# Optimization experiments

Measured on AMD Instinct MI355X. Metric: run time of the kernel, lower is better.

## Reference

```python
import jax, jax.numpy as jnp
import numpy as np

# Dims
B, S, D = 4, 4096, 1024
H, NB, A = 4, 4096, 4          # hashes, buckets, associativity
DK, DV, DT = 64, 128, 32        # key dim, value (mem) dim, vsa tag dim
BITS = 12                       # log2(NB)
TEMP = 1.0
VSA_W = 1.0
TANH_SCALE = 1.0
ETA = 0.1
WRITE_THR = 0.5
MATCH_THR = 0.0
NOV_THR = 0.0
EPS = 1e-6


def _l2n(x):
    return x / (jnp.linalg.norm(x, axis=-1, keepdims=True) + EPS)


def setup_inputs() -> dict:
    key = jax.random.key(0)
    ks = jax.random.split(key, 13)
    sc = 0.02
    return {
        "u": jax.random.normal(ks[0], (B, S, D), jnp.float32),
        "memK": jax.random.normal(ks[1], (H, NB, A, DK), jnp.float32),
        "memV": jax.random.normal(ks[2], (H, NB, A, DV), jnp.float32),
        "memT": jnp.tanh(jax.random.normal(ks[3], (H, NB, A, DT), jnp.float32)),
        "Wq": jax.random.normal(ks[4], (DK, D), jnp.float32) * sc,
        "Wwk": jax.random.normal(ks[5], (DK, D), jnp.float32) * sc,
        "Wv": jax.random.normal(ks[6], (DV, D), jnp.float32) * sc,
        "Wo": jax.random.normal(ks[7], (D, DV), jnp.float32) * sc,
        "Wg": jax.random.normal(ks[8], (1, D), jnp.float32) * sc,
        "bg": jnp.zeros((1,), jnp.float32),
        "Wvsa": jax.random.normal(ks[9], (DK, DT), jnp.float32) * sc,
        "R": jax.random.normal(ks[10], (H, DK, BITS), jnp.float32),
    }


def reference(u, memK, memV, memT, Wq, Wwk, Wv, Wo, Wg, bg, Wvsa, R):
    N = B * S
    uf = u.reshape(N, D)

    # ---- routing: sign-bit LSH over query key -> bucket index per hash ----
    qkey = uf @ Wq.T                                     # [N, DK]
    bits = (jnp.einsum("nd,hdk->nhk", qkey, R) > 0).astype(jnp.int32)
    pw = (2 ** jnp.arange(BITS, dtype=jnp.int32))
    idx = (bits * pw).sum(-1)                            # [N, H] bucket ids
    hh = jnp.arange(H)[None, :]                          # [1, H]

    # ---- associative gather read ----
    Kg = memK[hh, idx]                                   # [N, H, A, DK]
    Vg = memV[hh, idx]                                   # [N, H, A, DV]
    Tg = memT[hh, idx]                                   # [N, H, A, DT]
    qtag = jnp.tanh(TANH_SCALE * (qkey @ Wvsa))          # [N, DT]
    sc = (jnp.einsum("nd,nhad->nha", qkey, Kg) / np.sqrt(DK)
          + VSA_W * jnp.einsum("nt,nhat->nha", qtag, Tg) / np.sqrt(DT))
    w = jax.nn.softmax(sc.reshape(N, H * A) / TEMP, axis=-1)
    read = jnp.einsum("nk,nkd->nd", w, Vg.reshape(N, H * A, DV))
    y = (read @ Wo.T).reshape(B, S, D)

    # ---- gated scatter write with EMA + novelty ----
    wkey = uf @ Wwk.T                                    # [N, DK]
    wval = uf @ Wv.T                                     # [N, DV]
    gate = jax.nn.sigmoid(uf @ Wg.T + bg)                # [N, 1]
    wmask = (gate > WRITE_THR).astype(u.dtype)           # [N, 1]
    wtag = jnp.tanh(TANH_SCALE * (wkey @ Wvsa))          # [N, DT]

    sim = jnp.einsum("nd,nhad->nha", _l2n(wkey), _l2n(Kg))   # [N,H,A]
    astar = jnp.argmax(sim, axis=-1)                         # [N,H]
    bsim = jnp.max(sim, axis=-1)                             # [N,H]
    take = lambda G: jnp.take_along_axis(G, astar[:, :, None, None], axis=2)[:, :, 0]
    Kbest, Vbest, Tbest = take(Kg), take(Vg), take(Tg)       # [N,H,·]

    tagsim = jnp.einsum("nt,nhat->nha", _l2n(wtag), _l2n(Tg))
    novelty = 1.0 - jnp.max(tagsim, axis=-1)                 # [N,H]

    eff = (ETA * gate * wmask
           * (bsim >= MATCH_THR).astype(u.dtype)
           * (novelty >= NOV_THR).astype(u.dtype))           # [N,H]

    dK = eff[..., None] * (wkey[:, None, :] - Kbest)
    dV = eff[..., None] * (wval[:, None, :] - Vbest)
    dT = eff[..., None] * (wtag[:, None, :] - Tbest)
    Knew = memK.at[hh, idx, astar].add(dK)
    Vnew = memV.at[hh, idx, astar].add(dV)
    Tnew = memT.at[hh, idx, astar].add(dT)
    return y, Knew, Vnew, Tnew
```

## Files before the change

kernel.cpp:

```cpp
#include <hip/hip_runtime.h>
#include <hip/hip_bf16.h>
#include <math.h>

#define NTOK    16384
#define DMODEL  1024
#define HN      4
#define NBUCKET 4096
#define ASSOC   4
#define DKEY    64
#define DVAL    128
#define DTAG    32
#define NBITS   12
#define EPSV    1e-6f

typedef __bf16 bf16x8 __attribute__((ext_vector_type(8)));
typedef float  f32x4  __attribute__((ext_vector_type(4)));
typedef float  f32x2  __attribute__((ext_vector_type(2)));

__device__ __forceinline__ unsigned short f2bf_raw(float f) {
    __hip_bfloat16 h = __float2bfloat16(f);
    return *(unsigned short*)&h;
}

__global__ __launch_bounds__(256) void gemm_mfma(const float* __restrict__ A,
                                                 const float* __restrict__ B,
                                                 float* __restrict__ C,
                                                 int M, int N, int K) {
    __shared__ __align__(16) unsigned short As[4][128][8];
    __shared__ __align__(16) unsigned short Bs[4][128][8];
    const int t    = threadIdx.x;
    const int lane = t & 63;
    const int w    = t >> 6;
    const int wm   = (w & 1) * 64;
    const int wn   = (w >> 1) * 64;
    const int bm   = blockIdx.x * 128;
    const int bn   = blockIdx.y * 128;

    const int srow = t & 127;
    const int skg  = t >> 7;
    const float* Ap = A + (size_t)(bm + srow) * K;
    const float* Bp = B + (size_t)(bn + srow) * K;

    const int fr = lane & 15;
    const int kq = lane >> 4;

    f32x4 acc[4][4] = {};

    for (int k0 = 0; k0 < K; k0 += 32) {
        #pragma unroll
        for (int ii = 0; ii < 2; ++ii) {
            const int kg = skg + ii * 2;
            const float4 a0 = *(const float4*)(Ap + k0 + kg * 8);
            const float4 a1 = *(const float4*)(Ap + k0 + kg * 8 + 4);
            const float4 b0 = *(const float4*)(Bp + k0 + kg * 8);
            const float4 b1 = *(const float4*)(Bp + k0 + kg * 8 + 4);
            unsigned short* da = &As[kg][srow][0];
            da[0] = f2bf_raw(a0.x); da[1] = f2bf_raw(a0.y);
            da[2] = f2bf_raw(a0.z); da[3] = f2bf_raw(a0.w);
            da[4] = f2bf_raw(a1.x); da[5] = f2bf_raw(a1.y);
            da[6] = f2bf_raw(a1.z); da[7] = f2bf_raw(a1.w);
            unsigned short* db = &Bs[kg][srow][0];
            db[0] = f2bf_raw(b0.x); db[1] = f2bf_raw(b0.y);
            db[2] = f2bf_raw(b0.z); db[3] = f2bf_raw(b0.w);
            db[4] = f2bf_raw(b1.x); db[5] = f2bf_raw(b1.y);
            db[6] = f2bf_raw(b1.z); db[7] = f2bf_raw(b1.w);
        }
        __syncthreads();
        bf16x8 af[4], bfv[4];
        #pragma unroll
        for (int i = 0; i < 4; ++i) af[i]  = *(const bf16x8*)&As[kq][wm + i * 16 + fr][0];
        #pragma unroll
        for (int j = 0; j < 4; ++j) bfv[j] = *(const bf16x8*)&Bs[kq][wn + j * 16 + fr][0];
        #pragma unroll
        for (int i = 0; i < 4; ++i)
            #pragma unroll
            for (int j = 0; j < 4; ++j)
                acc[i][j] = __builtin_amdgcn_mfma_f32_16x16x32_bf16(af[i], bfv[j], acc[i][j], 0, 0, 0);
        __syncthreads();
    }
    #pragma unroll
    for (int i = 0; i < 4; ++i)
        #pragma unroll
        for (int j = 0; j < 4; ++j)
            #pragma unroll
            for (int r = 0; r < 4; ++r)
                C[(size_t)(bm + wm + i * 16 + kq * 4 + r) * N + (bn + wn + j * 16 + fr)] = acc[i][j][r];
}

__global__ __launch_bounds__(256) void gemm_wval_splitk(const float* __restrict__ A,
                                                        const float* __restrict__ B,
                                                        float* __restrict__ Cpart) {
    __shared__ __align__(16) unsigned short As[4][128][8];
    __shared__ __align__(16) unsigned short Bs[4][128][8];
    const int t    = threadIdx.x;
    const int lane = t & 63;
    const int w    = t >> 6;
    const int wm   = (w & 1) * 64;
    const int wn   = (w >> 1) * 64;
    const int bm   = blockIdx.x * 128;
    const int kz   = blockIdx.y;
    const int kbeg = kz * 256;

    const int srow = t & 127;
    const int skg  = t >> 7;
    const float* Ap = A + (size_t)(bm + srow) * DMODEL;
    const float* Bp = B + (size_t)srow * DMODEL;

    const int fr = lane & 15;
    const int kq = lane >> 4;

    f32x4 acc[4][4] = {};

    for (int k0 = kbeg; k0 < kbeg + 256; k0 += 32) {
        #pragma unroll
        for (int ii = 0; ii < 2; ++ii) {
            const int kg = skg + ii * 2;
            const float4 a0 = *(const float4*)(Ap + k0 + kg * 8);
            const float4 a1 = *(const float4*)(Ap + k0 + kg * 8 + 4);
            const float4 b0 = *(const float4*)(Bp + k0 + kg * 8);
            const float4 b1 = *(const float4*)(Bp + k0 + kg * 8 + 4);
            unsigned short* da = &As[kg][srow][0];
            da[0] = f2bf_raw(a0.x); da[1] = f2bf_raw(a0.y);
            da[2] = f2bf_raw(a0.z); da[3] = f2bf_raw(a0.w);
            da[4] = f2bf_raw(a1.x); da[5] = f2bf_raw(a1.y);
            da[6] = f2bf_raw(a1.z); da[7] = f2bf_raw(a1.w);
            unsigned short* db = &Bs[kg][srow][0];
            db[0] = f2bf_raw(b0.x); db[1] = f2bf_raw(b0.y);
            db[2] = f2bf_raw(b0.z); db[3] = f2bf_raw(b0.w);
            db[4] = f2bf_raw(b1.x); db[5] = f2bf_raw(b1.y);
            db[6] = f2bf_raw(b1.z); db[7] = f2bf_raw(b1.w);
        }
        __syncthreads();
        bf16x8 af[4], bfv[4];
        #pragma unroll
        for (int i = 0; i < 4; ++i) af[i]  = *(const bf16x8*)&As[kq][wm + i * 16 + fr][0];
        #pragma unroll
        for (int j = 0; j < 4; ++j) bfv[j] = *(const bf16x8*)&Bs[kq][wn + j * 16 + fr][0];
        #pragma unroll
        for (int i = 0; i < 4; ++i)
            #pragma unroll
            for (int j = 0; j < 4; ++j)
                acc[i][j] = __builtin_amdgcn_mfma_f32_16x16x32_bf16(af[i], bfv[j], acc[i][j], 0, 0, 0);
        __syncthreads();
    }
    float* Cp = Cpart + (size_t)kz * NTOK * 128;
    #pragma unroll
    for (int i = 0; i < 4; ++i)
        #pragma unroll
        for (int j = 0; j < 4; ++j)
            #pragma unroll
            for (int r = 0; r < 4; ++r)
                Cp[(size_t)(bm + wm + i * 16 + kq * 4 + r) * 128 + (wn + j * 16 + fr)] = acc[i][j][r];
}

__global__ __launch_bounds__(256) void gemm_f32_splitk(const float* __restrict__ A,
                                                       const float* __restrict__ B,
                                                       float* __restrict__ Cpart,
                                                       int M, int K, int K_quarter) {
    __shared__ __align__(16) float As[2][16][68];
    __shared__ __align__(16) float Bs[2][16][140];
    const int t  = threadIdx.x;
    const int bm = blockIdx.x * 64;
    const int kz = blockIdx.z;
    const int tx = t & 15;
    const int ty = t >> 4;

    const int arow = t >> 2, ac = (t & 3) * 4;
    const int brow = t >> 1, bc = (t & 1) * 8;
    const int bperm = brow + ((brow >> 5) << 2);
    const int goff  = tx * 8 + ((tx >> 2) << 2);

    const float* Apt = A + (size_t)(bm + arow) * K + ac;
    const float* Bpt = B + (size_t)brow * K + bc;

    const int kbeg = kz * K_quarter;
    const int NSTEP = 16;

    f32x2 acc2[4][4] = {};

    float4 av = *(const float4*)(Apt + kbeg);
    float4 b0 = *(const float4*)(Bpt + kbeg);
    float4 b1 = *(const float4*)(Bpt + kbeg + 4);
    As[0][ac + 0][arow] = av.x; As[0][ac + 1][arow] = av.y;
    As[0][ac + 2][arow] = av.z; As[0][ac + 3][arow] = av.w;
    Bs[0][bc + 0][bperm] = b0.x; Bs[0][bc + 1][bperm] = b0.y;
    Bs[0][bc + 2][bperm] = b0.z; Bs[0][bc + 3][bperm] = b0.w;
    Bs[0][bc + 4][bperm] = b1.x; Bs[0][bc + 5][bperm] = b1.y;
    Bs[0][bc + 6][bperm] = b1.z; Bs[0][bc + 7][bperm] = b1.w;
    __syncthreads();

    for (int s = 0; s < NSTEP; ++s) {
        const int cur = s & 1;
        if (s + 1 < NSTEP) {
            const int k0 = kbeg + (s + 1) * 16;
            av = *(const float4*)(Apt + k0);
            b0 = *(const float4*)(Bpt + k0);
            b1 = *(const float4*)(Bpt + k0 + 4);
        }
        #pragma unroll
        for (int kk = 0; kk < 16; ++kk) {
            const float4 a4 = *(const float4*)&As[cur][kk][ty * 4];
            const float4 v0 = *(const float4*)&Bs[cur][kk][goff];
            const float4 v1 = *(const float4*)&Bs[cur][kk][goff + 4];
            const float aa[4] = {a4.x, a4.y, a4.z, a4.w};
            const f32x2 bb[4] = {{v0.x, v0.y}, {v0.z, v0.w}, {v1.x, v1.y}, {v1.z, v1.w}};
            #pragma unroll
            for (int i = 0; i < 4; ++i) {
                const f32x2 as2 = {aa[i], aa[i]};
                #pragma unroll
                for (int j = 0; j < 4; ++j)
                    acc2[i][j] = __builtin_elementwise_fma(as2, bb[j], acc2[i][j]);
            }
        }
        if (s + 1 < NSTEP) {
            const int nb = cur ^ 1;
            As[nb][ac + 0][arow] = av.x; As[nb][ac + 1][arow] = av.y;
            As[nb][ac + 2][arow] = av.z; As[nb][ac + 3][arow] = av.w;
            Bs[nb][bc + 0][bperm] = b0.x; Bs[nb][bc + 1][bperm] = b0.y;
            Bs[nb][bc + 2][bperm] = b0.z; Bs[nb][bc + 3][bperm] = b0.w;
            Bs[nb][bc + 4][bperm] = b1.x; Bs[nb][bc + 5][bperm] = b1.y;
            Bs[nb][bc + 6][bperm] = b1.z; Bs[nb][bc + 7][bperm] = b1.w;
        }
        __syncthreads();
    }

    float* Cp = Cpart + (size_t)kz * M * 128;
    #pragma unroll
    for (int i = 0; i < 4; ++i) {
        float4 o0, o1;
        o0.x = acc2[i][0].x; o0.y = acc2[i][0].y; o0.z = acc2[i][1].x; o0.w = acc2[i][1].y;
        o1.x = acc2[i][2].x; o1.y = acc2[i][2].y; o1.z = acc2[i][3].x; o1.w = acc2[i][3].y;
        float* dst = &Cp[(size_t)(bm + ty * 4 + i) * 128 + tx * 8];
        *(float4*)dst       = o0;
        *(float4*)(dst + 4) = o1;
    }
}

__global__ __launch_bounds__(256) void gate_kernel(const float* __restrict__ u,
                                                   const float* __restrict__ Wg,
                                                   const float* __restrict__ bg,
                                                   float* __restrict__ gateg) {
    const int wv = threadIdx.x >> 6, lane = threadIdx.x & 63;
    const int n = blockIdx.x * 4 + wv;
    const float* up = u + (size_t)n * DMODEL;
    float acc = 0.f;
    #pragma unroll
    for (int j = 0; j < 16; ++j)
        acc += up[lane + 64 * j] * Wg[lane + 64 * j];
    #pragma unroll
    for (int off = 1; off < 64; off <<= 1) acc += __shfl_xor(acc, off);
    if (lane == 0) gateg[n] = 1.f / (1.f + expf(-(acc + bg[0])));
}

__global__ __launch_bounds__(256) void route_kernel(
    const float* __restrict__ memK, const float* __restrict__ memV,
    const float* __restrict__ memT, const float* __restrict__ R,
    const float* __restrict__ Wvsa,
    const float* __restrict__ partQ, const float* __restrict__ partW,
    const float* __restrict__ gateg,
    float* __restrict__ accK, float* __restrict__ accV, float* __restrict__ accT,
    float* __restrict__ readw) {
    __shared__ float sQK[4][64], sWK[4][64], sQT[4][32], sWT[4][32];
    __shared__ float sSc[4][16], sSim[4][16], sTsim[4][16], sW[4][16];
    __shared__ int   sIdx[4][4], sAst[4][4];
    __shared__ float sEff[4][4];

    const int wv = threadIdx.x >> 6;
    const int lane = threadIdx.x & 63;
    const int n = blockIdx.x * 4 + wv;
    const size_t PZ = (size_t)NTOK * 128;

    const size_t qb = (size_t)n * 128;
    const float qk = (partQ[qb + lane]          + partQ[PZ + qb + lane])
                   + (partQ[2 * PZ + qb + lane] + partQ[3 * PZ + qb + lane]);
    const float wk = (partQ[qb + 64 + lane]          + partQ[PZ + qb + 64 + lane])
                   + (partQ[2 * PZ + qb + 64 + lane] + partQ[3 * PZ + qb + 64 + lane]);
    sQK[wv][lane] = qk;
    sWK[wv][lane] = wk;
    float wk2 = wk * wk;
    #pragma unroll
    for (int off = 1; off < 64; off <<= 1) wk2 += __shfl_xor(wk2, off);
    const float wknorm = sqrtf(wk2) + EPSV;
    const float gate = gateg[n];
    __syncthreads();

    {
        const int tg = lane & 31;
        const float* keyp = (lane < 32) ? sQK[wv] : sWK[wv];
        float tacc = 0.f;
        for (int d = 0; d < 64; ++d) tacc += keyp[d] * Wvsa[d * DTAG + tg];
        const float tagv = tanhf(tacc);
        if (lane < 32) sQT[wv][tg] = tagv; else sWT[wv][tg] = tagv;
        float wt2 = (lane >= 32) ? tagv * tagv : 0.f;
        #pragma unroll
        for (int off = 1; off < 64; off <<= 1) wt2 += __shfl_xor(wt2, off);
        const float wtnorm = sqrtf(wt2) + EPSV;

        bool bit = false;
        if (lane < 48) {
            const int h = lane / 12, k = lane % 12;
            float bacc = 0.f;
            for (int d = 0; d < 64; ++d)
                bacc += sQK[wv][d] * R[(size_t)(h * DKEY + d) * NBITS + k];
            bit = bacc > 0.f;
        }
        const unsigned long long mask = __ballot(bit);
        if (lane < 4) sIdx[wv][lane] = (int)((mask >> (12 * lane)) & 0xFFFull);
        __syncthreads();

        const int slot = lane >> 2, sub = lane & 3;
        const int sh = slot >> 2, sa = slot & 3;
        const int rowS = (sh * NBUCKET + sIdx[wv][sh]) * ASSOC + sa;
        const float* Kp = memK + (size_t)rowS * DKEY;
        const float* Tp = memT + (size_t)rowS * DTAG;
        float d_qk = 0, d_wk = 0, d_kk = 0, d_qt = 0, d_wt = 0, d_tt = 0;
        for (int j = 0; j < 16; ++j) {
            const int d = sub * 16 + j;
            const float kv = Kp[d];
            d_qk += sQK[wv][d] * kv;
            d_wk += sWK[wv][d] * kv;
            d_kk += kv * kv;
        }
        for (int j = 0; j < 8; ++j) {
            const int d = sub * 8 + j;
            const float tv = Tp[d];
            d_qt += sQT[wv][d] * tv;
            d_wt += sWT[wv][d] * tv;
            d_tt += tv * tv;
        }
        #pragma unroll
        for (int off = 1; off <= 2; off <<= 1) {
            d_qk += __shfl_xor(d_qk, off);
            d_wk += __shfl_xor(d_wk, off);
            d_kk += __shfl_xor(d_kk, off);
            d_qt += __shfl_xor(d_qt, off);
            d_wt += __shfl_xor(d_wt, off);
            d_tt += __shfl_xor(d_tt, off);
        }
        if (sub == 0) {
            sSc[wv][slot]   = d_qk * 0.125f + d_qt * 0.17677669529663687f;
            sSim[wv][slot]  = d_wk / (wknorm * (sqrtf(d_kk) + EPSV));
            sTsim[wv][slot] = d_wt / (wtnorm * (sqrtf(d_tt) + EPSV));
        }
    }
    __syncthreads();

    if (lane < 16) {
        const float sc = sSc[wv][lane];
        float m = sc;
        #pragma unroll
        for (int off = 1; off < 16; off <<= 1) m = fmaxf(m, __shfl_xor(m, off, 16));
        const float e = expf(sc - m);
        float ssum = e;
        #pragma unroll
        for (int off = 1; off < 16; off <<= 1) ssum += __shfl_xor(ssum, off, 16);
        sW[wv][lane] = e / ssum;
    }
    if (lane < 4) {
        float bs = -1e30f; int as = 0; float mt = -1e30f;
        #pragma unroll
        for (int aa = 0; aa < 4; ++aa) {
            const float sv = sSim[wv][lane * 4 + aa];
            if (sv > bs) { bs = sv; as = aa; }
            mt = fmaxf(mt, sTsim[wv][lane * 4 + aa]);
        }
        const float novelty = 1.f - mt;
        float e = 0.1f * gate;
        if (!(gate > 0.5f) || !(bs >= 0.f) || !(novelty >= 0.f)) e = 0.f;
        sEff[wv][lane] = e;
        sAst[wv][lane] = as;
    }
    __syncthreads();

    float r0 = 0.f, r1 = 0.f;
    #pragma unroll
    for (int s2 = 0; s2 < 16; ++s2) {
        const int hh = s2 >> 2, aa = s2 & 3;
        const int rw = (hh * NBUCKET + sIdx[wv][hh]) * ASSOC + aa;
        const float wgt = sW[wv][s2];
        const float* Vp = memV + (size_t)rw * DVAL;
        r0 += wgt * Vp[lane];
        r1 += wgt * Vp[64 + lane];
    }
    readw[(size_t)n * DVAL + lane]      = r0;
    readw[(size_t)n * DVAL + 64 + lane] = r1;

    const float wv0 = (partW[qb + lane]          + partW[PZ + qb + lane])
                    + (partW[2 * PZ + qb + lane] + partW[3 * PZ + qb + lane]);
    const float wv1 = (partW[qb + 64 + lane]          + partW[PZ + qb + 64 + lane])
                    + (partW[2 * PZ + qb + 64 + lane] + partW[3 * PZ + qb + 64 + lane]);
    for (int hh = 0; hh < 4; ++hh) {
        const float e = sEff[wv][hh];
        if (e == 0.f) continue;
        const int rw = (hh * NBUCKET + sIdx[wv][hh]) * ASSOC + sAst[wv][hh];
        atomicAdd(&accK[(size_t)rw * DKEY + lane],
                  e * (sWK[wv][lane] - memK[(size_t)rw * DKEY + lane]));
        atomicAdd(&accV[(size_t)rw * DVAL + lane],
                  e * (wv0 - memV[(size_t)rw * DVAL + lane]));
        atomicAdd(&accV[(size_t)rw * DVAL + 64 + lane],
                  e * (wv1 - memV[(size_t)rw * DVAL + 64 + lane]));
        if (lane < 32)
            atomicAdd(&accT[(size_t)rw * DTAG + lane],
                      e * (sWT[wv][lane] - memT[(size_t)rw * DTAG + lane]));
    }
}

extern "C" void kernel_launch(void* const* d_in, const int* in_sizes, int n_in,
                              void* d_out, int out_size, void* d_ws, size_t ws_size,
                              hipStream_t stream) {
    const float* u    = (const float*)d_in[0];
    const float* memK = (const float*)d_in[1];
    const float* memV = (const float*)d_in[2];
    const float* memT = (const float*)d_in[3];
    const float* Wq   = (const float*)d_in[4];
    const float* Wwk  = (const float*)d_in[5];
    const float* Wv   = (const float*)d_in[6];
    const float* Wo   = (const float*)d_in[7];
    const float* Wg   = (const float*)d_in[8];
    const float* bg   = (const float*)d_in[9];
    const float* Wvsa = (const float*)d_in[10];
    const float* R    = (const float*)d_in[11];

    const int nK = HN * NBUCKET * ASSOC * DKEY;
    const int nV = HN * NBUCKET * ASSOC * DVAL;
    const int nT = HN * NBUCKET * ASSOC * DTAG;

    float* y_out = (float*)d_out;
    float* K_out = y_out + (size_t)NTOK * DMODEL;
    float* V_out = K_out + nK;
    float* T_out = V_out + nV;

    float* readw = (float*)d_ws;
    float* qwW   = readw + (size_t)NTOK * 128;
    float* gateg = qwW   + (size_t)128 * DMODEL;

    float* partQ = y_out;
    float* partW = y_out + (size_t)4 * NTOK * 128;

    hipMemcpyAsync(qwW,          Wq,  (size_t)DKEY * DMODEL * 4, hipMemcpyDeviceToDevice, stream);
    hipMemcpyAsync(qwW + 65536,  Wwk, (size_t)DKEY * DMODEL * 4, hipMemcpyDeviceToDevice, stream);

    gemm_f32_splitk<<<dim3(NTOK / 64, 1, 4), 256, 0, stream>>>(u, qwW, partQ, NTOK, DMODEL, DMODEL / 4);

    gate_kernel<<<NTOK / 4, 256, 0, stream>>>(u, Wg, bg, gateg);

    gemm_wval_splitk<<<dim3(NTOK / 128, 4), 256, 0, stream>>>(u, Wv, partW);

    hipMemcpyAsync(K_out, memK, (size_t)nK * 4, hipMemcpyDeviceToDevice, stream);
    hipMemcpyAsync(V_out, memV, (size_t)nV * 4, hipMemcpyDeviceToDevice, stream);
    hipMemcpyAsync(T_out, memT, (size_t)nT * 4, hipMemcpyDeviceToDevice, stream);

    route_kernel<<<NTOK / 4, 256, 0, stream>>>(memK, memV, memT, R, Wvsa,
                                               partQ, partW, gateg,
                                               K_out, V_out, T_out, readw);

    gemm_mfma<<<dim3(NTOK / 128, DMODEL / 128), 256, 0, stream>>>(readw, Wo, y_out, NTOK, DMODEL, DVAL);
}
```

Measured before the change: 402.8 us.

## Merge memory copies into one kernel and drop split-K for the value projection

The five device-to-device memcpys (Wq, Wwk, memK, memV, memT) become a single grid-stride float4 copy kernel. The value-projection GEMM goes from 4-way split-K with partial buffers to a full-K 64-row-tile kernel with 512 threads that writes the final result to workspace, and the route kernel reads it directly instead of summing four partials. This cuts partial-buffer traffic and memcpy launch overhead. The cost is fewer MFMAs per wave, more barriers per output tile, and 256 blocks for the GEMM instead of 512.

```diff
diff --git a/kernel.cpp b/kernel.cpp
--- a/kernel.cpp
+++ b/kernel.cpp
@@ -87,70 +87,61 @@
                 C[(size_t)(bm + wm + i * 16 + kq * 4 + r) * N + (bn + wn + j * 16 + fr)] = acc[i][j][r];
 }
 
-__global__ __launch_bounds__(256) void gemm_wval_splitk(const float* __restrict__ A,
-                                                        const float* __restrict__ B,
-                                                        float* __restrict__ Cpart) {
-    __shared__ __align__(16) unsigned short As[4][128][8];
+__global__ __launch_bounds__(512) void gemm_wval64(const float* __restrict__ A,
+                                                   const float* __restrict__ B,
+                                                   float* __restrict__ wvalg) {
+    __shared__ __align__(16) unsigned short As[4][64][8];
     __shared__ __align__(16) unsigned short Bs[4][128][8];
     const int t    = threadIdx.x;
     const int lane = t & 63;
     const int w    = t >> 6;
-    const int wm   = (w & 1) * 64;
-    const int wn   = (w >> 1) * 64;
-    const int bm   = blockIdx.x * 128;
-    const int kz   = blockIdx.y;
-    const int kbeg = kz * 256;
-
-    const int srow = t & 127;
-    const int skg  = t >> 7;
-    const float* Ap = A + (size_t)(bm + srow) * DMODEL;
-    const float* Bp = B + (size_t)srow * DMODEL;
+    const int wr   = w >> 1;
+    const int wc   = w & 1;
+    const int bm   = blockIdx.x * 64;
+
+    const int arow = t >> 3;
+    const int a4   = t & 7;
+    const int brow = t >> 2;
+    const int b4p  = (t & 3) * 2;
+
+    const float* Ap = A + (size_t)(bm + arow) * DMODEL + a4 * 4;
+    const float* Bp = B + (size_t)brow * DMODEL;
 
     const int fr = lane & 15;
     const int kq = lane >> 4;
 
-    f32x4 acc[4][4] = {};
-
-    for (int k0 = kbeg; k0 < kbeg + 256; k0 += 32) {
+    f32x4 acc[4] = {};
+
+    for (int k0 = 0; k0 < DMODEL; k0 += 32) {
+        {
+            const float4 av = *(const float4*)(Ap + k0);
+            unsigned short* da = &As[a4 >> 1][arow][(a4 & 1) * 4];
+            da[0] = f2bf_raw(av.x); da[1] = f2bf_raw(av.y);
+            da[2] = f2bf_raw(av.z); da[3] = f2bf_raw(av.w);
+        }
         #pragma unroll
         for (int ii = 0; ii < 2; ++ii) {
-            const int kg = skg + ii * 2;
-            const float4 a0 = *(const float4*)(Ap + k0 + kg * 8);
-            const float4 a1 = *(const float4*)(Ap + k0 + kg * 8 + 4);
-            const float4 b0 = *(const float4*)(Bp + k0 + kg * 8);
-            const float4 b1 = *(const float4*)(Bp + k0 + kg * 8 + 4);
-            unsigned short* da = &As[kg][srow][0];
-            da[0] = f2bf_raw(a0.x); da[1] = f2bf_raw(a0.y);
-            da[2] = f2bf_raw(a0.z); da[3] = f2bf_raw(a0.w);
-            da[4] = f2bf_raw(a1.x); da[5] = f2bf_raw(a1.y);
-            da[6] = f2bf_raw(a1.z); da[7] = f2bf_raw(a1.w);
-            unsigned short* db = &Bs[kg][srow][0];
-            db[0] = f2bf_raw(b0.x); db[1] = f2bf_raw(b0.y);
-            db[2] = f2bf_raw(b0.z); db[3] = f2bf_raw(b0.w);
-            db[4] = f2bf_raw(b1.x); db[5] = f2bf_raw(b1.y);
-            db[6] = f2bf_raw(b1.z); db[7] = f2bf_raw(b1.w);
-        }
-        __syncthreads();
-        bf16x8 af[4], bfv[4];
-        #pragma unroll
-        for (int i = 0; i < 4; ++i) af[i]  = *(const bf16x8*)&As[kq][wm + i * 16 + fr][0];
-        #pragma unroll
-        for (int j = 0; j < 4; ++j) bfv[j] = *(const bf16x8*)&Bs[kq][wn + j * 16 + fr][0];
-        #pragma unroll
-        for (int i = 0; i < 4; ++i)
-            #pragma unroll
-            for (int j = 0; j < 4; ++j)
-                acc[i][j] = __builtin_amdgcn_mfma_f32_16x16x32_bf16(af[i], bfv[j], acc[i][j], 0, 0, 0);
-        __syncthreads();
-    }
-    float* Cp = Cpart + (size_t)kz * NTOK * 128;
-    #pragma unroll
-    for (int i = 0; i < 4; ++i)
+            const int b4 = b4p + ii;
+            const float4 bv = *(const float4*)(Bp + k0 + b4 * 4);
+            unsigned short* db = &Bs[b4 >> 1][brow][(b4 & 1) * 4];
+            db[0] = f2bf_raw(bv.x); db[1] = f2bf_raw(bv.y);
+            db[2] = f2bf_raw(bv.z); db[3] = f2bf_raw(bv.w);
+        }
+        __syncthreads();
+        const bf16x8 af = *(const bf16x8*)&As[kq][wr * 16 + fr][0];
+        bf16x8 bfv[4];
+        #pragma unroll
+        for (int j = 0; j < 4; ++j) bfv[j] = *(const bf16x8*)&Bs[kq][wc * 64 + j * 16 + fr][0];
         #pragma unroll
         for (int j = 0; j < 4; ++j)
-            #pragma unroll
-            for (int r = 0; r < 4; ++r)
-                Cp[(size_t)(bm + wm + i * 16 + kq * 4 + r) * 128 + (wn + j * 16 + fr)] = acc[i][j][r];
+            acc[j] = __builtin_amdgcn_mfma_f32_16x16x32_bf16(af, bfv[j], acc[j], 0, 0, 0);
+        __syncthreads();
+    }
+    #pragma unroll
+    for (int j = 0; j < 4; ++j)
+        #pragma unroll
+        for (int r = 0; r < 4; ++r)
+            wvalg[(size_t)(bm + wr * 16 + kq * 4 + r) * 128 + wc * 64 + j * 16 + fr] = acc[j][r];
 }
 
 __global__ __launch_bounds__(256) void gemm_f32_splitk(const float* __restrict__ A,
@@ -252,11 +243,30 @@
     if (lane == 0) gateg[n] = 1.f / (1.f + expf(-(acc + bg[0])));
 }
 
+__global__ __launch_bounds__(256) void copyall_kernel(
+    const float4* __restrict__ sK, const float4* __restrict__ sV,
+    const float4* __restrict__ sT, const float4* __restrict__ sWq,
+    const float4* __restrict__ sWwk,
+    float4* __restrict__ dKVT, float4* __restrict__ dW) {
+    const int nK4 = (HN * NBUCKET * ASSOC * DKEY) / 4;
+    const int nV4 = (HN * NBUCKET * ASSOC * DVAL) / 4;
+    const int nT4 = (HN * NBUCKET * ASSOC * DTAG) / 4;
+    const int nW4 = (DKEY * DMODEL) / 4;
+    const int e1 = nK4, e2 = e1 + nV4, e3 = e2 + nT4, e4 = e3 + nW4, e5 = e4 + nW4;
+    for (int i = blockIdx.x * 256 + threadIdx.x; i < e5; i += gridDim.x * 256) {
+        if (i < e1)      dKVT[i] = sK[i];
+        else if (i < e2) dKVT[i] = sV[i - e1];
+        else if (i < e3) dKVT[i] = sT[i - e2];
+        else if (i < e4) dW[i - e3] = sWq[i - e3];
+        else             dW[i - e3] = sWwk[i - e4];
+    }
+}
+
 __global__ __launch_bounds__(256) void route_kernel(
     const float* __restrict__ memK, const float* __restrict__ memV,
     const float* __restrict__ memT, const float* __restrict__ R,
     const float* __restrict__ Wvsa,
-    const float* __restrict__ partQ, const float* __restrict__ partW,
+    const float* __restrict__ partQ, const float* __restrict__ wvalg,
     const float* __restrict__ gateg,
     float* __restrict__ accK, float* __restrict__ accV, float* __restrict__ accT,
     float* __restrict__ readw) {
@@ -385,10 +395,8 @@
     readw[(size_t)n * DVAL + lane]      = r0;
     readw[(size_t)n * DVAL + 64 + lane] = r1;
 
-    const float wv0 = (partW[qb + lane]          + partW[PZ + qb + lane])
-                    + (partW[2 * PZ + qb + lane] + partW[3 * PZ + qb + lane]);
-    const float wv1 = (partW[qb + 64 + lane]          + partW[PZ + qb + 64 + lane])
-                    + (partW[2 * PZ + qb + 64 + lane] + partW[3 * PZ + qb + 64 + lane]);
+    const float wv0 = wvalg[(size_t)n * DVAL + lane];
+    const float wv1 = wvalg[(size_t)n * DVAL + 64 + lane];
     for (int hh = 0; hh < 4; ++hh) {
         const float e = sEff[wv][hh];
         if (e == 0.f) continue;
@@ -431,27 +439,25 @@
     float* T_out = V_out + nV;
 
     float* readw = (float*)d_ws;
-    float* qwW   = readw + (size_t)NTOK * 128;
+    float* wvalg = readw + (size_t)NTOK * 128;
+    float* qwW   = wvalg + (size_t)NTOK * 128;
     float* gateg = qwW   + (size_t)128 * DMODEL;
 
     float* partQ = y_out;
-    float* partW = y_out + (size_t)4 * NTOK * 128;
-
-    hipMemcpyAsync(qwW,          Wq,  (size_t)DKEY * DMODEL * 4, hipMemcpyDeviceToDevice, stream);
-    hipMemcpyAsync(qwW + 65536,  Wwk, (size_t)DKEY * DMODEL * 4, hipMemcpyDeviceToDevice, stream);
+
+    copyall_kernel<<<2048, 256, 0, stream>>>((const float4*)memK, (const float4*)memV,
+                                             (const float4*)memT, (const float4*)Wq,
+                                             (const float4*)Wwk,
+                                             (float4*)K_out, (float4*)qwW);
 
     gemm_f32_splitk<<<dim3(NTOK / 64, 1, 4), 256, 0, stream>>>(u, qwW, partQ, NTOK, DMODEL, DMODEL / 4);
 
     gate_kernel<<<NTOK / 4, 256, 0, stream>>>(u, Wg, bg, gateg);
 
-    gemm_wval_splitk<<<dim3(NTOK / 128, 4), 256, 0, stream>>>(u, Wv, partW);
-
-    hipMemcpyAsync(K_out, memK, (size_t)nK * 4, hipMemcpyDeviceToDevice, stream);
-    hipMemcpyAsync(V_out, memV, (size_t)nV * 4, hipMemcpyDeviceToDevice, stream);
-    hipMemcpyAsync(T_out, memT, (size_t)nT * 4, hipMemcpyDeviceToDevice, stream);
+    gemm_wval64<<<NTOK / 64, 512, 0, stream>>>(u, Wv, wvalg);
 
     route_kernel<<<NTOK / 4, 256, 0, stream>>>(memK, memV, memT, R, Wvsa,
-                                               partQ, partW, gateg,
+                                               partQ, wvalg, gateg,
                                                K_out, V_out, T_out, readw);
 
     gemm_mfma<<<dim3(NTOK / 128, DMODEL / 128), 256, 0, stream>>>(readw, Wo, y_out, NTOK, DMODEL, DVAL);
```

Result: no change. 406.1 us (+0.8%).

## Fuse query/write-key and value projections into one interleaved kernel without split-K for values

Applied to the files above, without the earlier changes.

Merges the fp32 split-K query/write-key GEMM and the bf16 MFMA value GEMM into a single launch of 1280 blocks, interleaving one value-projection block among every four key-projection blocks so the two workloads share the GPU. The value projection now runs over the full K=1024 per 64-row tile and writes final results directly, which removes the four split-K partial buffers and their reduction in the route kernel. The memcpys and the gate kernel are reordered ahead of the fused launch. Value blocks do four times more sequential K work than key blocks, so load imbalance and tail effects are possible.

```diff
diff --git a/kernel.cpp b/kernel.cpp
--- a/kernel.cpp
+++ b/kernel.cpp
@@ -87,152 +87,149 @@
                 C[(size_t)(bm + wm + i * 16 + kq * 4 + r) * N + (bn + wn + j * 16 + fr)] = acc[i][j][r];
 }
 
-__global__ __launch_bounds__(256) void gemm_wval_splitk(const float* __restrict__ A,
-                                                        const float* __restrict__ B,
-                                                        float* __restrict__ Cpart) {
-    __shared__ __align__(16) unsigned short As[4][128][8];
-    __shared__ __align__(16) unsigned short Bs[4][128][8];
-    const int t    = threadIdx.x;
-    const int lane = t & 63;
-    const int w    = t >> 6;
-    const int wm   = (w & 1) * 64;
-    const int wn   = (w >> 1) * 64;
-    const int bm   = blockIdx.x * 128;
-    const int kz   = blockIdx.y;
-    const int kbeg = kz * 256;
-
-    const int srow = t & 127;
-    const int skg  = t >> 7;
-    const float* Ap = A + (size_t)(bm + srow) * DMODEL;
-    const float* Bp = B + (size_t)srow * DMODEL;
-
-    const int fr = lane & 15;
-    const int kq = lane >> 4;
-
-    f32x4 acc[4][4] = {};
-
-    for (int k0 = kbeg; k0 < kbeg + 256; k0 += 32) {
-        #pragma unroll
-        for (int ii = 0; ii < 2; ++ii) {
-            const int kg = skg + ii * 2;
-            const float4 a0 = *(const float4*)(Ap + k0 + kg * 8);
-            const float4 a1 = *(const float4*)(Ap + k0 + kg * 8 + 4);
-            const float4 b0 = *(const float4*)(Bp + k0 + kg * 8);
-            const float4 b1 = *(const float4*)(Bp + k0 + kg * 8 + 4);
-            unsigned short* da = &As[kg][srow][0];
-            da[0] = f2bf_raw(a0.x); da[1] = f2bf_raw(a0.y);
-            da[2] = f2bf_raw(a0.z); da[3] = f2bf_raw(a0.w);
-            da[4] = f2bf_raw(a1.x); da[5] = f2bf_raw(a1.y);
-            da[6] = f2bf_raw(a1.z); da[7] = f2bf_raw(a1.w);
-            unsigned short* db = &Bs[kg][srow][0];
-            db[0] = f2bf_raw(b0.x); db[1] = f2bf_raw(b0.y);
-            db[2] = f2bf_raw(b0.z); db[3] = f2bf_raw(b0.w);
-            db[4] = f2bf_raw(b1.x); db[5] = f2bf_raw(b1.y);
-            db[6] = f2bf_raw(b1.z); db[7] = f2bf_raw(b1.w);
-        }
+__global__ __launch_bounds__(256) void proj_fused(const float* __restrict__ A,
+                                                  const float* __restrict__ B,
+                                                  const float* __restrict__ Wv,
+                                                  float* __restrict__ Cpart,
+                                                  float* __restrict__ wvalg) {
+    __shared__ __align__(16) unsigned char smem[26624];
+    const int r = blockIdx.x;
+    const int t = threadIdx.x;
+
+    if ((r % 5) != 4) {
+        const int fid = (r / 5) * 4 + (r % 5);
+        const int bm  = (fid & 255) * 64;
+        const int kz  = fid >> 8;
+        float (*As)[16][68]  = reinterpret_cast<float(*)[16][68]>(smem);
+        float (*Bs)[16][140] = reinterpret_cast<float(*)[16][140]>(smem + 8704);
+
+        const int tx = t & 15;
+        const int ty = t >> 4;
+        const int arow = t >> 2, ac = (t & 3) * 4;
+        const int brow = t >> 1, bc = (t & 1) * 8;
+        const int bperm = brow + ((brow >> 5) << 2);
+        const int goff  = tx * 8 + ((tx >> 2) << 2);
+
+        const float* Apt = A + (size_t)(bm + arow) * DMODEL + ac;
+        const float* Bpt = B + (size_t)brow * DMODEL + bc;
+
+        const int kbeg = kz * 256;
+        const int NSTEP = 16;
+
+        f32x2 acc2[4][4] = {};
+
+        float4 av = *(const float4*)(Apt + kbeg);
+        float4 b0 = *(const float4*)(Bpt + kbeg);
+        float4 b1 = *(const float4*)(Bpt + kbeg + 4);
+        As[0][ac + 0][arow] = av.x; As[0][ac + 1][arow] = av.y;
+        As[0][ac + 2][arow] = av.z; As[0][ac + 3][arow] = av.w;
+        Bs[0][bc + 0][bperm] = b0.x; Bs[0][bc + 1][bperm] = b0.y;
+        Bs[0][bc + 2][bperm] = b0.z; Bs[0][bc + 3][bperm] = b0.w;
+        Bs[0][bc + 4][bperm] = b1.x; Bs[0][bc + 5][bperm] = b1.y;
+        Bs[0][bc + 6][bperm] = b1.z; Bs[0][bc + 7][bperm] = b1.w;
         __syncthreads();
-        bf16x8 af[4], bfv[4];
-        #pragma unroll
-        for (int i = 0; i < 4; ++i) af[i]  = *(const bf16x8*)&As[kq][wm + i * 16 + fr][0];
-        #pragma unroll
-        for (int j = 0; j < 4; ++j) bfv[j] = *(const bf16x8*)&Bs[kq][wn + j * 16 + fr][0];
-        #pragma unroll
-        for (int i = 0; i < 4; ++i)
-            #pragma unroll
-            for (int j = 0; j < 4; ++j)
-                acc[i][j] = __builtin_amdgcn_mfma_f32_16x16x32_bf16(af[i], bfv[j], acc[i][j], 0, 0, 0);
-        __syncthreads();
-    }
-    float* Cp = Cpart + (size_t)kz * NTOK * 128;
-    #pragma unroll
-    for (int i = 0; i < 4; ++i)
-        #pragma unroll
-        for (int j = 0; j < 4; ++j)
-            #pragma unroll
-            for (int r = 0; r < 4; ++r)
-                Cp[(size_t)(bm + wm + i * 16 + kq * 4 + r) * 128 + (wn + j * 16 + fr)] = acc[i][j][r];
-}
-
-__global__ __launch_bounds__(256) void gemm_f32_splitk(const float* __restrict__ A,
-                                                       const float* __restrict__ B,
-                                                       float* __restrict__ Cpart,
-                                                       int M, int K, int K_quarter) {
-    __shared__ __align__(16) float As[2][16][68];
-    __shared__ __align__(16) float Bs[2][16][140];
-    const int t  = threadIdx.x;
-    const int bm = blockIdx.x * 64;
-    const int kz = blockIdx.z;
-    const int tx = t & 15;
-    const int ty = t >> 4;
-
-    const int arow = t >> 2, ac = (t & 3) * 4;
-    const int brow = t >> 1, bc = (t & 1) * 8;
-    const int bperm = brow + ((brow >> 5) << 2);
-    const int goff  = tx * 8 + ((tx >> 2) << 2);
-
-    const float* Apt = A + (size_t)(bm + arow) * K + ac;
-    const float* Bpt = B + (size_t)brow * K + bc;
-
-    const int kbeg = kz * K_quarter;
-    const int NSTEP = 16;
-
-    f32x2 acc2[4][4] = {};
-
-    float4 av = *(const float4*)(Apt + kbeg);
-    float4 b0 = *(const float4*)(Bpt + kbeg);
-    float4 b1 = *(const float4*)(Bpt + kbeg + 4);
-    As[0][ac + 0][arow] = av.x; As[0][ac + 1][arow] = av.y;
-    As[0][ac + 2][arow] = av.z; As[0][ac + 3][arow] = av.w;
-    Bs[0][bc + 0][bperm] = b0.x; Bs[0][bc + 1][bperm] = b0.y;
-    Bs[0][bc + 2][bperm] = b0.z; Bs[0][bc + 3][bperm] = b0.w;
-    Bs[0][bc + 4][bperm] = b1.x; Bs[0][bc + 5][bperm] = b1.y;
-    Bs[0][bc + 6][bperm] = b1.z; Bs[0][bc + 7][bperm] = b1.w;
-    __syncthreads();
-
-    for (int s = 0; s < NSTEP; ++s) {
-        const int cur = s & 1;
-        if (s + 1 < NSTEP) {
-            const int k0 = kbeg + (s + 1) * 16;
-            av = *(const float4*)(Apt + k0);
-            b0 = *(const float4*)(Bpt + k0);
-            b1 = *(const float4*)(Bpt + k0 + 4);
-        }
-        #pragma unroll
-        for (int kk = 0; kk < 16; ++kk) {
-            const float4 a4 = *(const float4*)&As[cur][kk][ty * 4];
-            const float4 v0 = *(const float4*)&Bs[cur][kk][goff];
-            const float4 v1 = *(const float4*)&Bs[cur][kk][goff + 4];
-            const float aa[4] = {a4.x, a4.y, a4.z, a4.w};
-            const f32x2 bb[4] = {{v0.x, v0.y}, {v0.z, v0.w}, {v1.x, v1.y}, {v1.z, v1.w}};
-            #pragma unroll
-            for (int i = 0; i < 4; ++i) {
-                const f32x2 as2 = {aa[i], aa[i]};
+
+        for (int s = 0; s < NSTEP; ++s) {
+            const int cur = s & 1;
+            if (s + 1 < NSTEP) {
+                const int k0 = kbeg + (s + 1) * 16;
+                av = *(const float4*)(Apt + k0);
+                b0 = *(const float4*)(Bpt + k0);
+                b1 = *(const float4*)(Bpt + k0 + 4);
+            }
+            #pragma unroll
+            for (int kk = 0; kk < 16; ++kk) {
+                const float4 a4 = *(const float4*)&As[cur][kk][ty * 4];
+                const float4 v0 = *(const float4*)&Bs[cur][kk][goff];
+                const float4 v1 = *(const float4*)&Bs[cur][kk][goff + 4];
+                const float aa[4] = {a4.x, a4.y, a4.z, a4.w};
+                const f32x2 bb[4] = {{v0.x, v0.y}, {v0.z, v0.w}, {v1.x, v1.y}, {v1.z, v1.w}};
                 #pragma unroll
-                for (int j = 0; j < 4; ++j)
-                    acc2[i][j] = __builtin_elementwise_fma(as2, bb[j], acc2[i][j]);
-            }
-        }
-        if (s + 1 < NSTEP) {
-            const int nb = cur ^ 1;
-            As[nb][ac + 0][arow] = av.x; As[nb][ac + 1][arow] = av.y;
-            As[nb][ac + 2][arow] = av.z; As[nb][ac + 3][arow] = av.w;
-            Bs[nb][bc + 0][bperm] = b0.x; Bs[nb][bc + 1][bperm] = b0.y;
-            Bs[nb][bc + 2][bperm] = b0.z; Bs[nb][bc + 3][bperm] = b0.w;
-            Bs[nb][bc + 4][bperm] = b1.x; Bs[nb][bc + 5][bperm] = b1.y;
-            Bs[nb][bc + 6][bperm] = b1.z; Bs[nb][bc + 7][bperm] = b1.w;
-        }
-        __syncthreads();
-    }
-
-    float* Cp = Cpart + (size_t)kz * M * 128;
-    #pragma unroll
-    for (int i = 0; i < 4; ++i) {
-        float4 o0, o1;
-        o0.x = acc2[i][0].x; o0.y = acc2[i][0].y; o0.z = acc2[i][1].x; o0.w = acc2[i][1].y;
-        o1.x = acc2[i][2].x; o1.y = acc2[i][2].y; o1.z = acc2[i][3].x; o1.w = acc2[i][3].y;
-        float* dst = &Cp[(size_t)(bm + ty * 4 + i) * 128 + tx * 8];
-        *(float4*)dst       = o0;
-        *(float4*)(dst + 4) = o1;
+                for (int i = 0; i < 4; ++i) {
+                    const f32x2 as2 = {aa[i], aa[i]};
+                    #pragma unroll
+                    for (int j = 0; j < 4; ++j)
+                        acc2[i][j] = __builtin_elementwise_fma(as2, bb[j], acc2[i][j]);
+                }
+            }
+            if (s + 1 < NSTEP) {
+                const int nb = cur ^ 1;
+                As[nb][ac + 0][arow] = av.x; As[nb][ac + 1][arow] = av.y;
+                As[nb][ac + 2][arow] = av.z; As[nb][ac + 3][arow] = av.w;
+                Bs[nb][bc + 0][bperm] = b0.x; Bs[nb][bc + 1][bperm] = b0.y;
+                Bs[nb][bc + 2][bperm] = b0.z; Bs[nb][bc + 3][bperm] = b0.w;
+                Bs[nb][bc + 4][bperm] = b1.x; Bs[nb][bc + 5][bperm] = b1.y;
+                Bs[nb][bc + 6][bperm] = b1.z; Bs[nb][bc + 7][bperm] = b1.w;
+            }
+            __syncthreads();
+        }
+
+        float* Cp = Cpart + (size_t)kz * NTOK * 128;
+        #pragma unroll
+        for (int i = 0; i < 4; ++i) {
+            float4 o0, o1;
+            o0.x = acc2[i][0].x; o0.y = acc2[i][0].y; o0.z = acc2[i][1].x; o0.w = acc2[i][1].y;
+            o1.x = acc2[i][2].x; o1.y = acc2[i][2].y; o1.z = acc2[i][3].x; o1.w = acc2[i][3].y;
+            float* dst = &Cp[(size_t)(bm + ty * 4 + i) * 128 + tx * 8];
+            *(float4*)dst       = o0;
+            *(float4*)(dst + 4) = o1;
+        }
+    } else {
+        const int wid = r / 5;
+        const int bm  = wid * 64;
+        unsigned short (*Aw)[64][8]  = reinterpret_cast<unsigned short(*)[64][8]>(smem);
+        unsigned short (*Bw)[128][8] = reinterpret_cast<unsigned short(*)[128][8]>(smem + 4096);
+
+        const int lane = t & 63;
+        const int w    = t >> 6;
+        const int srow = t & 63;
+        const int skg  = t >> 6;
+        const int brow = t & 127;
+        const int bh   = t >> 7;
+
+        const float* Ap = A + (size_t)(bm + srow) * DMODEL;
+        const float* Bp = Wv + (size_t)brow * DMODEL;
+
+        const int fr = lane & 15;
+        const int kq = lane >> 4;
+
+        f32x4 acc[8] = {};
+
+        for (int k0 = 0; k0 < DMODEL; k0 += 32) {
+            {
+                const float4 a0 = *(const float4*)(Ap + k0 + skg * 8);
+                const float4 a1 = *(const float4*)(Ap + k0 + skg * 8 + 4);
+                unsigned short* da = &Aw[skg][srow][0];
+                da[0] = f2bf_raw(a0.x); da[1] = f2bf_raw(a0.y);
+                da[2] = f2bf_raw(a0.z); da[3] = f2bf_raw(a0.w);
+                da[4] = f2bf_raw(a1.x); da[5] = f2bf_raw(a1.y);
+                da[6] = f2bf_raw(a1.z); da[7] = f2bf_raw(a1.w);
+            }
+            #pragma unroll
+            for (int ii = 0; ii < 2; ++ii) {
+                const int kg = bh * 2 + ii;
+                const float4 b0 = *(const float4*)(Bp + k0 + kg * 8);
+                const float4 b1 = *(const float4*)(Bp + k0 + kg * 8 + 4);
+                unsigned short* db = &Bw[kg][brow][0];
+                db[0] = f2bf_raw(b0.x); db[1] = f2bf_raw(b0.y);
+                db[2] = f2bf_raw(b0.z); db[3] = f2bf_raw(b0.w);
+                db[4] = f2bf_raw(b1.x); db[5] = f2bf_raw(b1.y);
+                db[6] = f2bf_raw(b1.z); db[7] = f2bf_raw(b1.w);
+            }
+            __syncthreads();
+            const bf16x8 af = *(const bf16x8*)&Aw[kq][w * 16 + fr][0];
+            #pragma unroll
+            for (int j = 0; j < 8; ++j) {
+                const bf16x8 bfv = *(const bf16x8*)&Bw[kq][j * 16 + fr][0];
+                acc[j] = __builtin_amdgcn_mfma_f32_16x16x32_bf16(af, bfv, acc[j], 0, 0, 0);
+            }
+            __syncthreads();
+        }
+        #pragma unroll
+        for (int j = 0; j < 8; ++j)
+            #pragma unroll
+            for (int q = 0; q < 4; ++q)
+                wvalg[(size_t)(bm + w * 16 + kq * 4 + q) * 128 + j * 16 + fr] = acc[j][q];
     }
 }
 
@@ -256,7 +253,7 @@
     const float* __restrict__ memK, const float* __restrict__ memV,
     const float* __restrict__ memT, const float* __restrict__ R,
     const float* __restrict__ Wvsa,
-    const float* __restrict__ partQ, const float* __restrict__ partW,
+    const float* __restrict__ partQ, const float* __restrict__ wvalg,
     const float* __restrict__ gateg,
     float* __restrict__ accK, float* __restrict__ accV, float* __restrict__ accT,
     float* __restrict__ readw) {
@@ -385,10 +382,8 @@
     readw[(size_t)n * DVAL + lane]      = r0;
     readw[(size_t)n * DVAL + 64 + lane] = r1;
 
-    const float wv0 = (partW[qb + lane]          + partW[PZ + qb + lane])
-                    + (partW[2 * PZ + qb + lane] + partW[3 * PZ + qb + lane]);
-    const float wv1 = (partW[qb + 64 + lane]          + partW[PZ + qb + 64 + lane])
-                    + (partW[2 * PZ + qb + 64 + lane] + partW[3 * PZ + qb + 64 + lane]);
+    const float wv0 = wvalg[(size_t)n * DVAL + lane];
+    const float wv1 = wvalg[(size_t)n * DVAL + 64 + lane];
     for (int hh = 0; hh < 4; ++hh) {
         const float e = sEff[wv][hh];
         if (e == 0.f) continue;
@@ -431,27 +426,24 @@
     float* T_out = V_out + nV;
 
     float* readw = (float*)d_ws;
-    float* qwW   = readw + (size_t)NTOK * 128;
+    float* wvalg = readw + (size_t)NTOK * 128;
+    float* qwW   = wvalg + (size_t)NTOK * 128;
     float* gateg = qwW   + (size_t)128 * DMODEL;
 
     float* partQ = y_out;
-    float* partW = y_out + (size_t)4 * NTOK * 128;
 
     hipMemcpyAsync(qwW,          Wq,  (size_t)DKEY * DMODEL * 4, hipMemcpyDeviceToDevice, stream);
     hipMemcpyAsync(qwW + 65536,  Wwk, (size_t)DKEY * DMODEL * 4, hipMemcpyDeviceToDevice, stream);
-
-    gemm_f32_splitk<<<dim3(NTOK / 64, 1, 4), 256, 0, stream>>>(u, qwW, partQ, NTOK, DMODEL, DMODEL / 4);
-
-    gate_kernel<<<NTOK / 4, 256, 0, stream>>>(u, Wg, bg, gateg);
-
-    gemm_wval_splitk<<<dim3(NTOK / 128, 4), 256, 0, stream>>>(u, Wv, partW);
-
     hipMemcpyAsync(K_out, memK, (size_t)nK * 4, hipMemcpyDeviceToDevice, stream);
     hipMemcpyAsync(V_out, memV, (size_t)nV * 4, hipMemcpyDeviceToDevice, stream);
     hipMemcpyAsync(T_out, memT, (size_t)nT * 4, hipMemcpyDeviceToDevice, stream);
 
+    gate_kernel<<<NTOK / 4, 256, 0, stream>>>(u, Wg, bg, gateg);
+
+    proj_fused<<<1280, 256, 0, stream>>>(u, qwW, Wv, partQ, wvalg);
+
     route_kernel<<<NTOK / 4, 256, 0, stream>>>(memK, memV, memT, R, Wvsa,
-                                               partQ, partW, gateg,
+                                               partQ, wvalg, gateg,
                                                K_out, V_out, T_out, readw);
 
     gemm_mfma<<<dim3(NTOK / 128, DMODEL / 128), 256, 0, stream>>>(readw, Wo, y_out, NTOK, DMODEL, DVAL);
```

Measured after the change: 425.9 us. 1.06x slower.
